# Kernel tuning notes

Hardware: AMD Instinct MI355X
Metric: run time of the kernel (lower is better)

The kernel has to match this reference:

```python
import jax, jax.numpy as jnp
import numpy as np

H = 2048          # hidden_size
I = 2048          # per-expert intermediate = 6144 // (topk=2 + share=1)
E_ROUTED = 7      # num_experts - num_share_experts
NS = 1            # num_share_experts
TOPK = 2
TEMP = 1.0


def setup_inputs() -> dict:
    key = jax.random.key(0)
    ks = jax.random.split(key, 20)
    s = lambda fan_in: 1.0 / np.sqrt(fan_in)
    inp = {
        "x": jax.random.normal(ks[0], (4, 1024, H), dtype=jnp.float32),
        # router (nn.Linear(H, E_ROUTED)) + learnable gate bias (init zeros)
        "Wr": jax.random.normal(ks[1], (H, E_ROUTED), jnp.float32) * s(H),
        "br": jax.random.normal(ks[2], (E_ROUTED,), jnp.float32) * s(H),
        "gate_bias": jnp.zeros((E_ROUTED,), jnp.float32),
        # stacked routed-expert FFN params (up -> SwiGLU gate -> down)
        "Wup": jax.random.normal(ks[3], (E_ROUTED, H, I), jnp.float32) * s(H),
        "bup": jax.random.normal(ks[4], (E_ROUTED, I), jnp.float32) * s(H),
        "Wgate": jax.random.normal(ks[5], (E_ROUTED, I, I), jnp.float32) * s(I),
        "bgate": jax.random.normal(ks[6], (E_ROUTED, I), jnp.float32) * s(I),
        "Wdown": jax.random.normal(ks[7], (E_ROUTED, I, H), jnp.float32) * s(I),
        "bdown": jax.random.normal(ks[8], (E_ROUTED, H), jnp.float32) * s(I),
        # shared expert: share_up Linear(H, NS*I), SwiGLU(I), share_down Linear(I, H)
        "Wsu": jax.random.normal(ks[9], (H, NS * I), jnp.float32) * s(H),
        "bsu": jax.random.normal(ks[10], (NS * I,), jnp.float32) * s(H),
        "Wsg": jax.random.normal(ks[11], (I, I), jnp.float32) * s(I),
        "bsg": jax.random.normal(ks[12], (I,), jnp.float32) * s(I),
        "Wsd": jax.random.normal(ks[13], (I, H), jnp.float32) * s(I),
        "bsd": jax.random.normal(ks[14], (H,), jnp.float32) * s(I),
    }
    return inp


def _moe_forward(x, Wr, br, gate_bias, Wup, bup, Wgate, bgate, Wdown, bdown,
                 Wsu, bsu, Wsg, bsg, Wsd, bsd):
    B, S, _ = x.shape
    xt = x.reshape(-1, H)                                   # [N, H]
    N = xt.shape[0]

    # ---- router: top-k gating with scatter(-inf) + softmax over all routed experts
    gate = (xt @ Wr + br) / TEMP                            # [N, E]
    bias_gate = gate + gate_bias
    _, ids = jax.lax.top_k(bias_gate, TOPK)                 # [N, K]
    sel_logits = jnp.take_along_axis(gate, ids, axis=-1)    # [N, K] (unbiased logits)
    masked = jnp.full_like(gate, -jnp.inf)
    masked = masked.at[jnp.arange(N)[:, None], ids].set(sel_logits)
    probs = jax.nn.softmax(masked, axis=-1)                 # [N, E], zero off top-k

    # ---- routed experts: dense grouped FFN, combine weighted by probs
    # (probs are exactly 0 for unselected experts, matching the masked
    #  gather / scatter-add combine in the original loop)
    u = jnp.einsum('nh,ehi->eni', xt, Wup) + bup[:, None, :]            # [E, N, I]
    g = jax.nn.silu(jnp.einsum('eni,eij->enj', u, Wgate) + bgate[:, None, :]) * u
    eo = jnp.einsum('enj,ejh->enh', g, Wdown) + bdown[:, None, :]       # [E, N, H]
    out = jnp.einsum('ne,enh->nh', probs, eo)                           # [N, H]

    # ---- shared expert(s)
    su = (xt @ Wsu + bsu).reshape(N, NS, I)                 # [N, NS, I]
    sg = jax.nn.silu(su @ Wsg + bsg) * su                   # SwiGLU
    so = (sg @ Wsd + bsd).sum(axis=1)                       # [N, H]
    out = out + so

    return out.reshape(B, S, H)


def reference(x, Wr, br, gate_bias, Wup, bup, Wgate, bgate, Wdown, bdown,
              Wsu, bsu, Wsg, bsg, Wsd, bsd):
    return _moe_forward(x, Wr, br, gate_bias, Wup, bup, Wgate, bgate,
                        Wdown, bdown, Wsu, bsu, Wsg, bsg, Wsd, bsd)
```

## Files before the change

kernel.cpp:

```cpp
#include <hip/hip_runtime.h>
#include <stdint.h>

#define HD 2048
#define NTOK 4096
#define NROUTED 7
#define NEXP 8
#define ROWS_ROUTED 8192
#define ROWS_TOTAL 12288
#define ROWS_PAD 12416

typedef __attribute__((ext_vector_type(8))) __bf16 bf16x8;
typedef __attribute__((ext_vector_type(4))) float f32x4;
typedef __attribute__((ext_vector_type(8))) unsigned short u16x8;

__device__ __forceinline__ float bf2f(unsigned short h) {
  union { unsigned int u; float f; } x; x.u = ((unsigned int)h) << 16; return x.f;
}
__device__ __forceinline__ unsigned short f2bf(float f) {
  union { float f; unsigned int u; } x; x.f = f;
  unsigned int r = x.u + 0x7fffu + ((x.u >> 16) & 1u);
  return (unsigned short)(r >> 16);
}

__device__ __forceinline__ void async16(const void* g, void* l) {
  __builtin_amdgcn_global_load_lds(
      (__attribute__((address_space(1))) const void*)(uintptr_t)g,
      (__attribute__((address_space(3))) void*)(unsigned int)(uintptr_t)l,
      16, 0, 0);
}

__global__ __launch_bounds__(256) void k_convert_bf16(const float* __restrict__ in,
                                                      unsigned short* __restrict__ out, int n) {
  int i = (blockIdx.x * 256 + threadIdx.x) * 4;
  if (i >= n) return;
  float4 v = *(const float4*)(in + i);
  ushort4 o; o.x = f2bf(v.x); o.y = f2bf(v.y); o.z = f2bf(v.z); o.w = f2bf(v.w);
  *(ushort4*)(out + i) = o;
}

__global__ __launch_bounds__(256) void k_transpose_bf16(const float* __restrict__ in,
                                                        unsigned short* __restrict__ out) {
  __shared__ float tile[32][33];
  const size_t bs = (size_t)HD * HD;
  in += (size_t)blockIdx.z * bs; out += (size_t)blockIdx.z * bs;
  int x = threadIdx.x & 31, y = threadIdx.x >> 5;
  int r0 = blockIdx.y * 32, c0 = blockIdx.x * 32;
  #pragma unroll
  for (int i = 0; i < 4; i++) tile[y + 8*i][x] = in[(size_t)(r0 + y + 8*i) * HD + c0 + x];
  __syncthreads();
  #pragma unroll
  for (int i = 0; i < 4; i++) out[(size_t)(c0 + y + 8*i) * HD + r0 + x] = f2bf(tile[x][y + 8*i]);
}

__global__ __launch_bounds__(256) void k_router(const float* __restrict__ x, const float* __restrict__ Wr,
                                                const float* __restrict__ br, const float* __restrict__ gbias,
                                                int* __restrict__ ids, float* __restrict__ wts,
                                                int* __restrict__ ctrl) {
  int lane = threadIdx.x & 63, wid = threadIdx.x >> 6;
  int t = blockIdx.x * 4 + wid;
  const float* xr = x + (size_t)t * HD;
  float acc[NROUTED];
  #pragma unroll
  for (int e = 0; e < NROUTED; e++) acc[e] = 0.f;
  for (int k = lane; k < HD; k += 64) {
    float xv = xr[k];
    const float* wrow = Wr + k * NROUTED;
    #pragma unroll
    for (int e = 0; e < NROUTED; e++) acc[e] += xv * wrow[e];
  }
  #pragma unroll
  for (int e = 0; e < NROUTED; e++) {
    #pragma unroll
    for (int off = 32; off > 0; off >>= 1) acc[e] += __shfl_down(acc[e], off);
  }
  if (lane == 0) {
    float lg[NROUTED], bg[NROUTED];
    #pragma unroll
    for (int e = 0; e < NROUTED; e++) { lg[e] = acc[e] + br[e]; bg[e] = lg[e] + gbias[e]; }
    int i1 = 0;
    #pragma unroll
    for (int e = 1; e < NROUTED; e++) if (bg[e] > bg[i1]) i1 = e;
    int i2 = (i1 == 0) ? 1 : 0;
    #pragma unroll
    for (int e = 0; e < NROUTED; e++) if (e != i1 && bg[e] > bg[i2]) i2 = e;
    float l1 = lg[i1], l2 = lg[i2];
    float m = fmaxf(l1, l2);
    float p1 = __expf(l1 - m), p2 = __expf(l2 - m);
    float s = p1 + p2;
    ids[2*t] = i1; ids[2*t+1] = i2;
    wts[2*t] = p1 / s; wts[2*t+1] = p2 / s;
    atomicAdd(&ctrl[i1], 1); atomicAdd(&ctrl[i2], 1);
  }
}

__global__ void k_offsets(int* ctrl) {
  if (threadIdx.x == 0 && blockIdx.x == 0) {
    ctrl[7] = NTOK;
    int o = 0;
    #pragma unroll
    for (int e = 0; e < NEXP; e++) { ctrl[8 + e] = o; o += ctrl[e]; }
  }
}

__global__ __launch_bounds__(256) void k_build_lists(const int* __restrict__ ids, int* __restrict__ ctrl,
                                                     int* __restrict__ tok_list, int* __restrict__ tok_pos) {
  int t = blockIdx.x * 256 + threadIdx.x;
  if (t >= NTOK) return;
  #pragma unroll
  for (int j = 0; j < 2; j++) {
    int e = ids[2*t + j];
    int pos = ctrl[8 + e] + atomicAdd(&ctrl[16 + e], 1);
    tok_list[pos] = t;
    tok_pos[2*t + j] = pos;
  }
  tok_list[ROWS_ROUTED + t] = t;
}

template<int MODE>
__global__ __launch_bounds__(256) void k_moe_gemm(
    const unsigned short* __restrict__ Abase,
    const unsigned short* __restrict__ WTr,
    const unsigned short* __restrict__ WTs,
    const float* __restrict__ biasR,
    const float* __restrict__ biasS,
    const int* __restrict__ ctrl,
    const int* __restrict__ tok_list,
    const unsigned short* __restrict__ Uep,
    unsigned short* __restrict__ Out)
{
  const int e   = blockIdx.z;
  const int cnt = ctrl[e];
  const int m0  = blockIdx.y * 128;
  if (m0 >= cnt) return;
  const int off = ctrl[8 + e];
  const int n0  = blockIdx.x * 128;

  const unsigned short* W = (e < NROUTED) ? (WTr + (size_t)e * HD * HD) : WTs;
  const float* bias = (e < NROUTED) ? (biasR + e * HD) : biasS;

  __shared__ __align__(16) unsigned short As[128 * 32];
  __shared__ __align__(16) unsigned short Bs[128 * 32];

  const int tid  = threadIdx.x;
  const int lane = tid & 63;
  const int wid  = tid >> 6;

  const int srow = tid >> 2;
  const int skel = (tid & 3) * 8;

  int ar0 = m0 + srow, ar1 = m0 + 64 + srow;
  size_t ga0, ga1;
  if (MODE == 0) {
    int c1 = cnt - 1;
    int t0 = tok_list[off + (ar0 < cnt ? ar0 : c1)];
    int t1 = tok_list[off + (ar1 < cnt ? ar1 : c1)];
    ga0 = (size_t)t0 * HD; ga1 = (size_t)t1 * HD;
  } else {
    ga0 = (size_t)(off + ar0) * HD; ga1 = (size_t)(off + ar1) * HD;
  }
  const unsigned short* pA0 = Abase + ga0 + skel;
  const unsigned short* pA1 = Abase + ga1 + skel;
  const unsigned short* pB0 = W + (size_t)(n0 + srow) * HD + skel;
  const unsigned short* pB1 = W + (size_t)(n0 + 64 + srow) * HD + skel;

  unsigned short* lA0 = As + wid * 512;
  unsigned short* lA1 = As + 2048 + wid * 512;
  unsigned short* lB0 = Bs + wid * 512;
  unsigned short* lB1 = Bs + 2048 + wid * 512;

  const int wm = (wid >> 1) * 64;
  const int wn = (wid & 1) * 64;
  const int rm = lane & 15;
  const int kq = (lane >> 4) * 8;

  f32x4 zero = {0.f, 0.f, 0.f, 0.f};
  f32x4 acc[4][4];
  #pragma unroll
  for (int i = 0; i < 4; i++)
    #pragma unroll
    for (int j = 0; j < 4; j++) acc[i][j] = zero;

  for (int k0 = 0; k0 < HD; k0 += 32) {
    __syncthreads();
    async16(pA0, lA0); async16(pA1, lA1);
    async16(pB0, lB0); async16(pB1, lB1);
    pA0 += 32; pA1 += 32; pB0 += 32; pB1 += 32;
    __syncthreads();
    bf16x8 af[4], bfr[4];
    #pragma unroll
    for (int mi = 0; mi < 4; mi++) af[mi]  = *(const bf16x8*)(As + (wm + mi*16 + rm) * 32 + kq);
    #pragma unroll
    for (int ni = 0; ni < 4; ni++) bfr[ni] = *(const bf16x8*)(Bs + (wn + ni*16 + rm) * 32 + kq);
    #pragma unroll
    for (int mi = 0; mi < 4; mi++)
      #pragma unroll
      for (int ni = 0; ni < 4; ni++)
        acc[mi][ni] = __builtin_amdgcn_mfma_f32_16x16x32_bf16(af[mi], bfr[ni], acc[mi][ni], 0, 0, 0);
  }

  const int quad = lane >> 4;
  #pragma unroll
  for (int mi = 0; mi < 4; mi++) {
    int rb = wm + mi * 16 + quad * 4;
    #pragma unroll
    for (int r = 0; r < 4; r++) {
      int gm = m0 + rb + r;
      if (gm < cnt) {
        size_t orow = (size_t)(off + gm) * HD;
        #pragma unroll
        for (int ni = 0; ni < 4; ni++) {
          int gn = n0 + wn + ni * 16 + rm;
          float v = acc[mi][ni][r] + bias[gn];
          if (MODE == 1) {
            float uv = bf2f(Uep[orow + gn]);
            float sg = v / (1.f + __expf(-v));
            v = sg * uv;
          }
          Out[orow + gn] = f2bf(v);
        }
      }
    }
  }
}

__global__ __launch_bounds__(256) void k_combine(const unsigned short* __restrict__ eo,
                                                 const int* __restrict__ tok_pos,
                                                 const float* __restrict__ wts,
                                                 float* __restrict__ out) {
  int t = blockIdx.x;
  int h = threadIdx.x * 8;
  int p0 = tok_pos[2*t], p1 = tok_pos[2*t+1];
  float w0 = wts[2*t], w1 = wts[2*t+1];
  u16x8 a = *(const u16x8*)(eo + (size_t)p0 * HD + h);
  u16x8 b = *(const u16x8*)(eo + (size_t)p1 * HD + h);
  u16x8 c = *(const u16x8*)(eo + (size_t)(ROWS_ROUTED + t) * HD + h);
  float* o = out + (size_t)t * HD + h;
  #pragma unroll
  for (int i = 0; i < 8; i++) o[i] = w0 * bf2f(a[i]) + w1 * bf2f(b[i]) + bf2f(c[i]);
}

extern "C" void kernel_launch(void* const* d_in, const int* in_sizes, int n_in,
                              void* d_out, int out_size, void* d_ws, size_t ws_size,
                              hipStream_t stream) {
  (void)in_sizes; (void)n_in; (void)out_size; (void)ws_size;
  const float* x     = (const float*)d_in[0];
  const float* Wr    = (const float*)d_in[1];
  const float* br    = (const float*)d_in[2];
  const float* gbias = (const float*)d_in[3];
  const float* Wup   = (const float*)d_in[4];
  const float* bup   = (const float*)d_in[5];
  const float* Wgate = (const float*)d_in[6];
  const float* bgate = (const float*)d_in[7];
  const float* Wdown = (const float*)d_in[8];
  const float* bdown = (const float*)d_in[9];
  const float* Wsu   = (const float*)d_in[10];
  const float* bsu   = (const float*)d_in[11];
  const float* Wsg   = (const float*)d_in[12];
  const float* bsg   = (const float*)d_in[13];
  const float* Wsd   = (const float*)d_in[14];
  const float* bsd   = (const float*)d_in[15];
  float* out = (float*)d_out;

  char* ws = (char*)d_ws;
  size_t o = 0;
  auto alloc = [&](size_t bytes) { char* p = ws + o; o += (bytes + 255) & ~(size_t)255; return p; };
  unsigned short* WT_r = (unsigned short*)alloc((size_t)7 * HD * HD * 2);
  unsigned short* WT_s = (unsigned short*)alloc((size_t)HD * HD * 2);
  unsigned short* xbf  = (unsigned short*)alloc((size_t)NTOK * HD * 2);
  unsigned short* bufU = (unsigned short*)alloc((size_t)ROWS_PAD * HD * 2);
  unsigned short* bufG = (unsigned short*)alloc((size_t)ROWS_PAD * HD * 2);
  int*   ctrl     = (int*)alloc(4096);
  int*   ids      = (int*)alloc(NTOK * 2 * 4);
  float* wts      = (float*)alloc(NTOK * 2 * 4);
  int*   tok_list = (int*)alloc(ROWS_TOTAL * 4);
  int*   tok_pos  = (int*)alloc(NTOK * 2 * 4);

  hipMemsetAsync(ctrl, 0, 96, stream);
  k_convert_bf16<<<NTOK * HD / 1024, 256, 0, stream>>>(x, xbf, NTOK * HD);
  k_router<<<NTOK / 4, 256, 0, stream>>>(x, Wr, br, gbias, ids, wts, ctrl);
  k_offsets<<<1, 64, 0, stream>>>(ctrl);
  k_build_lists<<<NTOK / 256, 256, 0, stream>>>(ids, ctrl, tok_list, tok_pos);

  dim3 tgrid(HD / 32, HD / 32, 7), tgrid1(HD / 32, HD / 32, 1);
  dim3 ggrid(HD / 128, 32, 8);

  k_transpose_bf16<<<tgrid, 256, 0, stream>>>(Wup, WT_r);
  k_transpose_bf16<<<tgrid1, 256, 0, stream>>>(Wsu, WT_s);
  k_moe_gemm<0><<<ggrid, 256, 0, stream>>>(xbf, WT_r, WT_s, bup, bsu, ctrl, tok_list, nullptr, bufU);

  k_transpose_bf16<<<tgrid, 256, 0, stream>>>(Wgate, WT_r);
  k_transpose_bf16<<<tgrid1, 256, 0, stream>>>(Wsg, WT_s);
  k_moe_gemm<1><<<ggrid, 256, 0, stream>>>(bufU, WT_r, WT_s, bgate, bsg, ctrl, tok_list, bufU, bufG);

  k_transpose_bf16<<<tgrid, 256, 0, stream>>>(Wdown, WT_r);
  k_transpose_bf16<<<tgrid1, 256, 0, stream>>>(Wsd, WT_s);
  k_moe_gemm<2><<<ggrid, 256, 0, stream>>>(bufG, WT_r, WT_s, bdown, bsd, ctrl, tok_list, nullptr, bufU);

  k_combine<<<NTOK, 256, 0, stream>>>(bufU, tok_pos, wts, out);
}
```

Before: 1.100 ms.

## Double GEMM K-tile with XOR-swizzled LDS and merge weight transposes

The grouped MoE GEMM now stages 64-wide K slices instead of 32, which halves the number of barrier pairs per tile. An XOR swizzle on the LDS chunk index is meant to avoid bank conflicts on the fragment reads. The weight transpose uses 64x64 tiles with float4 loads and ushort4 stores, and handles routed and shared experts in one launch writing a single contiguous 8-expert buffer. The cost is twice the LDS per block, which may lower occupancy, and the GEMM still runs without double buffering.

```diff
diff --git a/kernel.cpp b/kernel.cpp
--- a/kernel.cpp
+++ b/kernel.cpp
@@ -38,18 +38,35 @@
   *(ushort4*)(out + i) = o;
 }
 
-__global__ __launch_bounds__(256) void k_transpose_bf16(const float* __restrict__ in,
-                                                        unsigned short* __restrict__ out) {
-  __shared__ float tile[32][33];
+__global__ __launch_bounds__(256) void k_transpose8(const float* __restrict__ Wr_,
+                                                    const float* __restrict__ Ws_,
+                                                    unsigned short* __restrict__ out) {
+  __shared__ float tile[64][65];
   const size_t bs = (size_t)HD * HD;
-  in += (size_t)blockIdx.z * bs; out += (size_t)blockIdx.z * bs;
-  int x = threadIdx.x & 31, y = threadIdx.x >> 5;
-  int r0 = blockIdx.y * 32, c0 = blockIdx.x * 32;
-  #pragma unroll
-  for (int i = 0; i < 4; i++) tile[y + 8*i][x] = in[(size_t)(r0 + y + 8*i) * HD + c0 + x];
+  int z = blockIdx.z;
+  const float* in = (z < NROUTED) ? (Wr_ + (size_t)z * bs) : Ws_;
+  unsigned short* dst = out + (size_t)z * bs;
+  const int t = threadIdx.x;
+  const int r0 = blockIdx.y * 64, c0 = blockIdx.x * 64;
+  const int lr = t >> 4;
+  const int lc = (t & 15) * 4;
+  #pragma unroll
+  for (int p = 0; p < 4; p++) {
+    int row = p * 16 + lr;
+    float4 v = *(const float4*)(in + (size_t)(r0 + row) * HD + c0 + lc);
+    tile[row][lc] = v.x; tile[row][lc+1] = v.y; tile[row][lc+2] = v.z; tile[row][lc+3] = v.w;
+  }
   __syncthreads();
   #pragma unroll
-  for (int i = 0; i < 4; i++) out[(size_t)(c0 + y + 8*i) * HD + r0 + x] = f2bf(tile[x][y + 8*i]);
+  for (int p = 0; p < 4; p++) {
+    int oc = p * 16 + lr;
+    ushort4 o;
+    o.x = f2bf(tile[lc+0][oc]);
+    o.y = f2bf(tile[lc+1][oc]);
+    o.z = f2bf(tile[lc+2][oc]);
+    o.w = f2bf(tile[lc+3][oc]);
+    *(ushort4*)(dst + (size_t)(c0 + oc) * HD + r0 + lc) = o;
+  }
 }
 
 __global__ __launch_bounds__(256) void k_router(const float* __restrict__ x, const float* __restrict__ Wr,
@@ -119,8 +136,7 @@
 template<int MODE>
 __global__ __launch_bounds__(256) void k_moe_gemm(
     const unsigned short* __restrict__ Abase,
-    const unsigned short* __restrict__ WTr,
-    const unsigned short* __restrict__ WTs,
+    const unsigned short* __restrict__ WT,
     const float* __restrict__ biasR,
     const float* __restrict__ biasS,
     const int* __restrict__ ctrl,
@@ -135,43 +151,51 @@
   const int off = ctrl[8 + e];
   const int n0  = blockIdx.x * 128;
 
-  const unsigned short* W = (e < NROUTED) ? (WTr + (size_t)e * HD * HD) : WTs;
+  const unsigned short* W = WT + (size_t)e * HD * HD;
   const float* bias = (e < NROUTED) ? (biasR + e * HD) : biasS;
 
-  __shared__ __align__(16) unsigned short As[128 * 32];
-  __shared__ __align__(16) unsigned short Bs[128 * 32];
+  __shared__ __align__(16) unsigned short As[128 * 64];
+  __shared__ __align__(16) unsigned short Bs[128 * 64];
 
   const int tid  = threadIdx.x;
   const int lane = tid & 63;
   const int wid  = tid >> 6;
 
-  const int srow = tid >> 2;
-  const int skel = (tid & 3) * 8;
-
-  int ar0 = m0 + srow, ar1 = m0 + 64 + srow;
-  size_t ga0, ga1;
-  if (MODE == 0) {
-    int c1 = cnt - 1;
-    int t0 = tok_list[off + (ar0 < cnt ? ar0 : c1)];
-    int t1 = tok_list[off + (ar1 < cnt ? ar1 : c1)];
-    ga0 = (size_t)t0 * HD; ga1 = (size_t)t1 * HD;
-  } else {
-    ga0 = (size_t)(off + ar0) * HD; ga1 = (size_t)(off + ar1) * HD;
-  }
-  const unsigned short* pA0 = Abase + ga0 + skel;
-  const unsigned short* pA1 = Abase + ga1 + skel;
-  const unsigned short* pB0 = W + (size_t)(n0 + srow) * HD + skel;
-  const unsigned short* pB1 = W + (size_t)(n0 + 64 + srow) * HD + skel;
-
-  unsigned short* lA0 = As + wid * 512;
-  unsigned short* lA1 = As + 2048 + wid * 512;
-  unsigned short* lB0 = Bs + wid * 512;
-  unsigned short* lB1 = Bs + 2048 + wid * 512;
+  const int srow   = tid >> 3;
+  const int gchunk = (tid & 7) ^ (srow & 7);
+  const int skel   = gchunk * 8;
+
+  size_t ga[4];
+  #pragma unroll
+  for (int r = 0; r < 4; r++) {
+    int ar = m0 + srow + 32 * r;
+    if (MODE == 0) {
+      int tkn = tok_list[off + (ar < cnt ? ar : cnt - 1)];
+      ga[r] = (size_t)tkn * HD;
+    } else {
+      ga[r] = (size_t)(off + ar) * HD;
+    }
+  }
+  const unsigned short* pA[4];
+  const unsigned short* pB[4];
+  #pragma unroll
+  for (int r = 0; r < 4; r++) {
+    pA[r] = Abase + ga[r] + skel;
+    pB[r] = W + (size_t)(n0 + srow + 32 * r) * HD + skel;
+  }
+
+  unsigned short* lA[4]; unsigned short* lB[4];
+  #pragma unroll
+  for (int r = 0; r < 4; r++) {
+    lA[r] = As + (32 * r + 8 * wid) * 64;
+    lB[r] = Bs + (32 * r + 8 * wid) * 64;
+  }
 
   const int wm = (wid >> 1) * 64;
   const int wn = (wid & 1) * 64;
   const int rm = lane & 15;
-  const int kq = (lane >> 4) * 8;
+  const int cquad = lane >> 4;
+  const int rx = rm & 7;
 
   f32x4 zero = {0.f, 0.f, 0.f, 0.f};
   f32x4 acc[4][4];
@@ -180,22 +204,27 @@
     #pragma unroll
     for (int j = 0; j < 4; j++) acc[i][j] = zero;
 
-  for (int k0 = 0; k0 < HD; k0 += 32) {
+  for (int k0 = 0; k0 < HD; k0 += 64) {
     __syncthreads();
-    async16(pA0, lA0); async16(pA1, lA1);
-    async16(pB0, lB0); async16(pB1, lB1);
-    pA0 += 32; pA1 += 32; pB0 += 32; pB1 += 32;
+    #pragma unroll
+    for (int r = 0; r < 4; r++) { async16(pA[r], lA[r]); async16(pB[r], lB[r]); }
+    #pragma unroll
+    for (int r = 0; r < 4; r++) { pA[r] += 64; pB[r] += 64; }
     __syncthreads();
-    bf16x8 af[4], bfr[4];
-    #pragma unroll
-    for (int mi = 0; mi < 4; mi++) af[mi]  = *(const bf16x8*)(As + (wm + mi*16 + rm) * 32 + kq);
-    #pragma unroll
-    for (int ni = 0; ni < 4; ni++) bfr[ni] = *(const bf16x8*)(Bs + (wn + ni*16 + rm) * 32 + kq);
-    #pragma unroll
-    for (int mi = 0; mi < 4; mi++)
+    #pragma unroll
+    for (int kg = 0; kg < 2; kg++) {
+      const int slot = ((cquad + 4 * kg) ^ rx) * 8;
+      bf16x8 af[4], bfr[4];
       #pragma unroll
-      for (int ni = 0; ni < 4; ni++)
-        acc[mi][ni] = __builtin_amdgcn_mfma_f32_16x16x32_bf16(af[mi], bfr[ni], acc[mi][ni], 0, 0, 0);
+      for (int mi = 0; mi < 4; mi++) af[mi]  = *(const bf16x8*)(As + (wm + mi*16 + rm) * 64 + slot);
+      #pragma unroll
+      for (int ni = 0; ni < 4; ni++) bfr[ni] = *(const bf16x8*)(Bs + (wn + ni*16 + rm) * 64 + slot);
+      #pragma unroll
+      for (int mi = 0; mi < 4; mi++)
+        #pragma unroll
+        for (int ni = 0; ni < 4; ni++)
+          acc[mi][ni] = __builtin_amdgcn_mfma_f32_16x16x32_bf16(af[mi], bfr[ni], acc[mi][ni], 0, 0, 0);
+    }
   }
 
   const int quad = lane >> 4;
@@ -264,8 +293,7 @@
   char* ws = (char*)d_ws;
   size_t o = 0;
   auto alloc = [&](size_t bytes) { char* p = ws + o; o += (bytes + 255) & ~(size_t)255; return p; };
-  unsigned short* WT_r = (unsigned short*)alloc((size_t)7 * HD * HD * 2);
-  unsigned short* WT_s = (unsigned short*)alloc((size_t)HD * HD * 2);
+  unsigned short* WT   = (unsigned short*)alloc((size_t)8 * HD * HD * 2);
   unsigned short* xbf  = (unsigned short*)alloc((size_t)NTOK * HD * 2);
   unsigned short* bufU = (unsigned short*)alloc((size_t)ROWS_PAD * HD * 2);
   unsigned short* bufG = (unsigned short*)alloc((size_t)ROWS_PAD * HD * 2);
@@ -281,20 +309,17 @@
   k_offsets<<<1, 64, 0, stream>>>(ctrl);
   k_build_lists<<<NTOK / 256, 256, 0, stream>>>(ids, ctrl, tok_list, tok_pos);
 
-  dim3 tgrid(HD / 32, HD / 32, 7), tgrid1(HD / 32, HD / 32, 1);
+  dim3 tgrid(HD / 64, HD / 64, 8);
   dim3 ggrid(HD / 128, 32, 8);
 
-  k_transpose_bf16<<<tgrid, 256, 0, stream>>>(Wup, WT_r);
-  k_transpose_bf16<<<tgrid1, 256, 0, stream>>>(Wsu, WT_s);
-  k_moe_gemm<0><<<ggrid, 256, 0, stream>>>(xbf, WT_r, WT_s, bup, bsu, ctrl, tok_list, nullptr, bufU);
-
-  k_transpose_bf16<<<tgrid, 256, 0, stream>>>(Wgate, WT_r);
-  k_transpose_bf16<<<tgrid1, 256, 0, stream>>>(Wsg, WT_s);
-  k_moe_gemm<1><<<ggrid, 256, 0, stream>>>(bufU, WT_r, WT_s, bgate, bsg, ctrl, tok_list, bufU, bufG);
-
-  k_transpose_bf16<<<tgrid, 256, 0, stream>>>(Wdown, WT_r);
-  k_transpose_bf16<<<tgrid1, 256, 0, stream>>>(Wsd, WT_s);
-  k_moe_gemm<2><<<ggrid, 256, 0, stream>>>(bufG, WT_r, WT_s, bdown, bsd, ctrl, tok_list, nullptr, bufU);
+  k_transpose8<<<tgrid, 256, 0, stream>>>(Wup, Wsu, WT);
+  k_moe_gemm<0><<<ggrid, 256, 0, stream>>>(xbf, WT, bup, bsu, ctrl, tok_list, nullptr, bufU);
+
+  k_transpose8<<<tgrid, 256, 0, stream>>>(Wgate, Wsg, WT);
+  k_moe_gemm<1><<<ggrid, 256, 0, stream>>>(bufU, WT, bgate, bsg, ctrl, tok_list, bufU, bufG);
+
+  k_transpose8<<<tgrid, 256, 0, stream>>>(Wdown, Wsd, WT);
+  k_moe_gemm<2><<<ggrid, 256, 0, stream>>>(bufG, WT, bdown, bsd, ctrl, tok_list, nullptr, bufU);
 
   k_combine<<<NTOK, 256, 0, stream>>>(bufU, tok_pos, wts, out);
 }
```

After: 1.102 ms. Within noise of the previous version (+0.1%).
